# Optimization experiments

Hardware: AMD Instinct MI355X
Metric: run time of the kernel (lower is better)

The kernel has to match this reference:

```python
import jax, jax.numpy as jnp
import numpy as np
from jax import lax

N, M, T, V, C_IN, C_OUT, KT, PAD = 16, 2, 300, 25, 64, 64, 9, 4
BN_EPS = 1e-5

# NTU-RGB+D 25-joint skeleton edges (0-indexed), symmetric, plus self-loops
_NTU_EDGES = [(0,1),(1,20),(2,20),(3,2),(4,20),(5,4),(6,5),(7,6),(8,20),(9,8),
              (10,9),(11,10),(12,0),(13,12),(14,13),(15,14),(16,0),(17,16),
              (18,17),(19,18),(21,22),(22,7),(23,24),(24,11)]

def _build_adj():
    A = np.zeros((V, V), dtype=np.float32)
    for i, j in _NTU_EDGES:
        A[i, j] = 1.0
        A[j, i] = 1.0
    A += np.eye(V, dtype=np.float32)  # self-loops (DGL GCN preprocessing)
    return jnp.asarray(A)


def setup_inputs() -> dict:
    key = jax.random.key(0)
    ks = jax.random.split(key, 8)
    stdv = 1.0 / np.sqrt(C_OUT)
    # conv_init: normal(0, sqrt(2/(out_channels*prod(kernel))))
    conv_std = np.sqrt(2.0 / (C_OUT * KT * 1))
    return {
        "h": jax.random.normal(ks[0], (N * M * T * V, C_IN), dtype=jnp.float32),
        "adj": _build_adj(),
        "gcn_w": jax.random.uniform(ks[1], (C_IN, C_OUT), minval=-stdv, maxval=stdv, dtype=jnp.float32),
        "gcn_b": jax.random.uniform(ks[2], (C_OUT,), minval=-stdv, maxval=stdv, dtype=jnp.float32),
        "conv_w": conv_std * jax.random.normal(ks[3], (C_OUT, C_OUT, KT, 1), dtype=jnp.float32),
        "conv_b": jnp.zeros((C_OUT,), dtype=jnp.float32),
        "bn_gamma": jnp.ones((C_OUT,), dtype=jnp.float32),
        "bn_beta": jnp.zeros((C_OUT,), dtype=jnp.float32),
        "bn_mean": 0.1 * jax.random.normal(ks[4], (C_OUT,), dtype=jnp.float32),
        "bn_var": jax.random.uniform(ks[5], (C_OUT,), minval=0.5, maxval=1.5, dtype=jnp.float32),
    }


def reference(h, adj, gcn_w, gcn_b, conv_w, conv_b, bn_gamma, bn_beta, bn_mean, bn_var):
    # ---- GCNLayer (dropout is identity at eval) ----
    # symmetric norm = deg^{-1/2}, identical across the N*M*T copies of the skeleton
    norm = adj.sum(axis=1) ** -0.5                      # (V,)
    x = h @ gcn_w                                        # (N*M*T*V, C_OUT)
    x = x.reshape(-1, V, C_OUT) * norm[:, None]          # pre-norm scale
    x = jnp.einsum('vu,buc->bvc', adj, x)                # copy_src + sum aggregation
    x = x * norm[:, None] + gcn_b                        # post-norm scale + bias
    x = jax.nn.relu(x)

    # ---- TemporalConvNetwork ----
    v = x.reshape(N, M, T, V, C_OUT)
    v = v.transpose(0, 1, 4, 2, 3).reshape(N * M, C_OUT, T, V)   # (NM, C, T, V)
    v = lax.conv_general_dilated(v, conv_w, window_strides=(1, 1),
                                 padding=[(PAD, PAD), (0, 0)],
                                 dimension_numbers=('NCHW', 'OIHW', 'NCHW'))
    v = v + conv_b[None, :, None, None]
    inv_std = bn_gamma / jnp.sqrt(bn_var + BN_EPS)       # eval-mode BatchNorm2d
    v = (v - bn_mean[None, :, None, None]) * inv_std[None, :, None, None] + bn_beta[None, :, None, None]
    v = jax.nn.relu(v)
    v = v.reshape(N, M, C_OUT, T, V).transpose(0, 1, 3, 4, 2)    # (N, M, T, V, C)

    # ---- residual (downt is None since in_feats == out_feats and stride == 1) ----
    return v + h.reshape(N, M, T, V, C_IN)
```

## Files before the change

kernel.cpp:

```cpp
#include <hip/hip_runtime.h>
#include <hip/hip_bf16.h>


typedef __bf16 bf16x8 __attribute__((ext_vector_type(8)));
typedef __bf16 bf16x4 __attribute__((ext_vector_type(4)));
typedef float  f32x4  __attribute__((ext_vector_type(4)));

#define Y_OFF   0
#define WC2_OFF 30720000
#define WGT_OFF 30793728
#define A2P_OFF 30801920
#define SC_OFF  30803968
#define SH_OFF  30804224

__global__ __launch_bounds__(256) void prep_kernel(
    const float* __restrict__ adj, const float* __restrict__ gcn_w,
    const float* __restrict__ conv_w, const float* __restrict__ conv_b,
    const float* __restrict__ bn_g, const float* __restrict__ bn_b,
    const float* __restrict__ bn_m, const float* __restrict__ bn_v,
    __bf16* __restrict__ wc2, __bf16* __restrict__ wgt,
    __bf16* __restrict__ a2p, float* __restrict__ scale, float* __restrict__ shift) {
  int tid = threadIdx.x;
  for (int e = blockIdx.x * 256 + tid; e < 36864; e += gridDim.x * 256) {
    int j = e & 7, t1 = e >> 3, c = t1 & 63, g = t1 >> 6;
    int kap = g * 8 + j, kt = kap >> 6, ci = kap & 63;
    wc2[e] = (__bf16)conv_w[(c * 64 + ci) * 9 + kt];
  }
  if (blockIdx.x == 0) {
    for (int e = tid; e < 4096; e += 256) {
      int c = e >> 6, k = e & 63;
      wgt[e] = (__bf16)gcn_w[k * 64 + c];
    }
  } else if (blockIdx.x == 1) {
    for (int e = tid; e < 1024; e += 256) {
      int v = e >> 5, u = e & 31;
      float val = 0.f;
      if (v < 25 && u < 25) {
        float dv = 0.f, du = 0.f;
        for (int t = 0; t < 25; ++t) { dv += adj[v * 25 + t]; du += adj[u * 25 + t]; }
        val = rsqrtf(dv) * adj[v * 25 + u] * rsqrtf(du);
      }
      a2p[e] = (__bf16)val;
    }
  } else if (blockIdx.x == 2) {
    if (tid < 64) {
      float sc = bn_g[tid] * rsqrtf(bn_v[tid] + 1e-5f);
      scale[tid] = sc;
      shift[tid] = (conv_b[tid] - bn_m[tid]) * sc + bn_b[tid];
    }
  }
}

__global__ __launch_bounds__(64) void gcn_kernel(
    const float* __restrict__ h, const __bf16* __restrict__ wgt_g,
    const __bf16* __restrict__ a2p_g, const float* __restrict__ gcn_b,
    __bf16* __restrict__ y) {
  __shared__ __align__(16) __bf16 hb[2048];
  __shared__ __align__(16) __bf16 x1t[64 * 40];
  int lane = threadIdx.x;
  int l15 = lane & 15, quad = lane >> 4;
  int skel = blockIdx.x;
  int nm = skel / 300, tloc = skel - nm * 300;

  bf16x8 awg[4][2];
  for (int mt = 0; mt < 4; ++mt)
    for (int kk = 0; kk < 2; ++kk)
      awg[mt][kk] = *(const bf16x8*)&wgt_g[(mt * 16 + l15) * 64 + kk * 32 + quad * 8];
  bf16x8 ba[2];
  for (int nt = 0; nt < 2; ++nt)
    ba[nt] = *(const bf16x8*)&a2p_g[(nt * 16 + l15) * 32 + quad * 8];

  if (lane < 56) *(uint4*)&hb[1600 + lane * 8] = (uint4){0u, 0u, 0u, 0u};
  for (int it = 0; it < 7; ++it) {
    int u = it * 4 + quad;
    if (u < 25) {
      float4 hv = *(const float4*)&h[(skel * 25 + u) * 64 + l15 * 4];
      bf16x4 b4; b4[0] = (__bf16)hv.x; b4[1] = (__bf16)hv.y; b4[2] = (__bf16)hv.z; b4[3] = (__bf16)hv.w;
      int ch = l15 >> 1;
      *(bf16x4*)&hb[u * 64 + (((ch ^ (u & 7)) * 8) | ((l15 & 1) * 4))] = b4;
    }
  }
  for (int mt = 0; mt < 4; ++mt)
    for (int nt = 0; nt < 2; ++nt) {
      f32x4 acc = {0.f, 0.f, 0.f, 0.f};
      int u = nt * 16 + l15;
      for (int kk = 0; kk < 2; ++kk) {
        bf16x8 b = *(const bf16x8*)&hb[u * 64 + (((kk * 4 + quad) ^ (u & 7)) * 8)];
        acc = __builtin_amdgcn_mfma_f32_16x16x32_bf16(awg[mt][kk], b, acc, 0, 0, 0);
      }
      int c0 = mt * 16 + quad * 4;
      for (int r = 0; r < 4; ++r) x1t[(c0 + r) * 40 + u] = (__bf16)acc[r];
    }
  for (int mt = 0; mt < 4; ++mt)
    for (int nt = 0; nt < 2; ++nt) {
      f32x4 acc = {0.f, 0.f, 0.f, 0.f};
      bf16x8 a = *(const bf16x8*)&x1t[(mt * 16 + l15) * 40 + quad * 8];
      acc = __builtin_amdgcn_mfma_f32_16x16x32_bf16(a, ba[nt], acc, 0, 0, 0);
      int v = nt * 16 + l15, c0 = mt * 16 + quad * 4;
      if (v < 25) {
        float4 bias = *(const float4*)&gcn_b[c0];
        bf16x4 o;
        o[0] = (__bf16)fmaxf(acc[0] + bias.x, 0.f);
        o[1] = (__bf16)fmaxf(acc[1] + bias.y, 0.f);
        o[2] = (__bf16)fmaxf(acc[2] + bias.z, 0.f);
        o[3] = (__bf16)fmaxf(acc[3] + bias.w, 0.f);
        int ch = (c0 >> 3) ^ (v & 7);
        *(bf16x4*)&hb[v * 64 + ((ch * 8) | (c0 & 7))] = o;
      }
    }
  for (int e = lane; e < 200; e += 64) {
    int v = e >> 3, ch = e & 7;
    uint4 val = *(const uint4*)&hb[v * 64 + ((ch ^ (v & 7)) * 8)];
    *(uint4*)&y[((nm * 25 + v) * 300 + tloc) * 64 + ch * 8] = val;
  }
}

__global__ __launch_bounds__(256, 8) void conv_kernel(
    const __bf16* __restrict__ y, const __bf16* __restrict__ wc2,
    const float* __restrict__ scale, const float* __restrict__ shift,
    const float* __restrict__ h, float* __restrict__ out) {
  __shared__ __align__(16) __bf16 my[72 * 64];
  int tid = threadIdx.x, w = tid >> 6, lane = tid & 63;
  int l15 = lane & 15, quad = lane >> 4;
  int ti = blockIdx.x, vv = blockIdx.y, nm = blockIdx.z;
  int t0 = (ti < 4) ? ti * 64 : 236;

  {
    const __bf16* ybase = &y[((nm * 25 + vv) * 300) * 64];
    uint4 stg[3];
    for (int it = 0; it < 3; ++it) {
      int idx = it * 256 + tid;
      uint4 val = {0u, 0u, 0u, 0u};
      if (idx < 576) {
        int r = idx >> 3, ch = idx & 7, tg = t0 - 4 + r;
        if (tg >= 0 && tg < 300) val = *(const uint4*)&ybase[tg * 64 + ch * 8];
      }
      stg[it] = val;
    }
    for (int it = 0; it < 3; ++it) {
      int idx = it * 256 + tid;
      if (idx < 576) {
        int r = idx >> 3, ch = idx & 7;
        *(uint4*)&my[r * 64 + ((ch ^ (r & 7)) * 8)] = stg[it];
      }
    }
  }
  __syncthreads();

  f32x4 acc[4];
  for (int n = 0; n < 4; ++n) acc[n] = (f32x4){0.f, 0.f, 0.f, 0.f};

  bf16x8 a0, a1;
#define LOADA(dst, kk_) dst = *(const bf16x8*)&wc2[((((kk_) * 4 + quad) * 64) + w * 16 + l15) * 8];
#define COMPUTE(kk_, areg) { int kt = (kk_) >> 1, chb = ((kk_) & 1) * 4 + quad; \
    for (int n = 0; n < 4; ++n) { \
      int row = n * 16 + l15 + kt; \
      bf16x8 b = *(const bf16x8*)&my[row * 64 + ((chb ^ (row & 7)) * 8)]; \
      acc[n] = __builtin_amdgcn_mfma_f32_16x16x32_bf16(areg, b, acc[n], 0, 0, 0); \
    } }
  LOADA(a0, 0)
  for (int kk = 0; kk < 18; kk += 2) {
    LOADA(a1, kk + 1)
    COMPUTE(kk, a0)
    if (kk + 2 < 18) LOADA(a0, kk + 2)
    COMPUTE(kk + 1, a1)
  }
#undef LOADA
#undef COMPUTE

  int c0 = w * 16 + quad * 4;
  float4 sc = *(const float4*)&scale[c0];
  float4 sh = *(const float4*)&shift[c0];
  for (int n = 0; n < 4; ++n) {
    int tt = t0 + n * 16 + l15;
    int idx = ((nm * 300 + tt) * 25 + vv) * 64 + c0;
    float4 hr = *(const float4*)&h[idx];
    float4 o;
    o.x = fmaxf(acc[n][0] * sc.x + sh.x, 0.f) + hr.x;
    o.y = fmaxf(acc[n][1] * sc.y + sh.y, 0.f) + hr.y;
    o.z = fmaxf(acc[n][2] * sc.z + sh.z, 0.f) + hr.z;
    o.w = fmaxf(acc[n][3] * sc.w + sh.w, 0.f) + hr.w;
    *(float4*)&out[idx] = o;
  }
}

extern "C" void kernel_launch(void* const* d_in, const int* in_sizes, int n_in,
                              void* d_out, int out_size, void* d_ws, size_t ws_size,
                              hipStream_t stream) {
  const float* h      = (const float*)d_in[0];
  const float* adj    = (const float*)d_in[1];
  const float* gcn_w  = (const float*)d_in[2];
  const float* gcn_b  = (const float*)d_in[3];
  const float* conv_w = (const float*)d_in[4];
  const float* conv_b = (const float*)d_in[5];
  const float* bn_g   = (const float*)d_in[6];
  const float* bn_b   = (const float*)d_in[7];
  const float* bn_m   = (const float*)d_in[8];
  const float* bn_v   = (const float*)d_in[9];
  float* out = (float*)d_out;
  char* ws = (char*)d_ws;

  __bf16* y_ws   = (__bf16*)(ws + Y_OFF);
  __bf16* wc2    = (__bf16*)(ws + WC2_OFF);
  __bf16* wgt    = (__bf16*)(ws + WGT_OFF);
  __bf16* a2p    = (__bf16*)(ws + A2P_OFF);
  float*  scale  = (float*)(ws + SC_OFF);
  float*  shift  = (float*)(ws + SH_OFF);

  prep_kernel<<<64, 256, 0, stream>>>(adj, gcn_w, conv_w, conv_b, bn_g, bn_b, bn_m, bn_v,
                                      wc2, wgt, a2p, scale, shift);
  gcn_kernel<<<9600, 64, 0, stream>>>(h, wgt, a2p, gcn_b, y_ws);
  conv_kernel<<<dim3(5, 25, 32), 256, 0, stream>>>(y_ws, wc2, scale, shift, h, out);
}
```

Measured before the change: 173.8 us.

## Switch temporal conv to 32x32x16 MFMA tiles with two waves per block

Rewrites the temporal conv kernel to use 32x32x16 bf16 MFMA instead of 16x16x32. Each block now runs two waves instead of four, and each wave computes 32 channels by 64 timesteps. The packed conv weight layout in the prep kernel is reordered to match the new A-operand fragment. The aim is fewer MFMA issues and fewer LDS B-fragment reads per output, at the cost of more accumulator registers per thread and fewer threads per block for staging loads. The epilogue now writes strided float4 groups of channels, which changes how the global accesses coalesce.

```diff
diff --git a/kernel.cpp b/kernel.cpp
--- a/kernel.cpp
+++ b/kernel.cpp
@@ -5,6 +5,7 @@
 typedef __bf16 bf16x8 __attribute__((ext_vector_type(8)));
 typedef __bf16 bf16x4 __attribute__((ext_vector_type(4)));
 typedef float  f32x4  __attribute__((ext_vector_type(4)));
+typedef float  f32x16 __attribute__((ext_vector_type(16)));
 
 #define Y_OFF   0
 #define WC2_OFF 30720000
@@ -23,7 +24,8 @@
   int tid = threadIdx.x;
   for (int e = blockIdx.x * 256 + tid; e < 36864; e += gridDim.x * 256) {
     int j = e & 7, t1 = e >> 3, c = t1 & 63, g = t1 >> 6;
-    int kap = g * 8 + j, kt = kap >> 6, ci = kap & 63;
+    int kt = g >> 3, ks = (g >> 1) & 3, hi = g & 1;
+    int ci = ks * 16 + hi * 8 + j;
     wc2[e] = (__bf16)conv_w[(c * 64 + ci) * 9 + kt];
   }
   if (blockIdx.x == 0) {
@@ -115,21 +117,41 @@
   }
 }
 
-__global__ __launch_bounds__(256, 8) void conv_kernel(
+__device__ __forceinline__ void conv_epilogue(
+    const f32x16& a, int tt, int nm, int vv, int cbase,
+    const float* __restrict__ scale, const float* __restrict__ shift,
+    const float* __restrict__ h, float* __restrict__ out) {
+  int base = ((nm * 300 + tt) * 25 + vv) * 64 + cbase;
+#pragma unroll
+  for (int q = 0; q < 4; ++q) {
+    int idx = base + q * 8;
+    float4 hr = *(const float4*)&h[idx];
+    float4 s4 = *(const float4*)&scale[cbase + q * 8];
+    float4 h4 = *(const float4*)&shift[cbase + q * 8];
+    float4 o;
+    o.x = fmaxf(a[q * 4 + 0] * s4.x + h4.x, 0.f) + hr.x;
+    o.y = fmaxf(a[q * 4 + 1] * s4.y + h4.y, 0.f) + hr.y;
+    o.z = fmaxf(a[q * 4 + 2] * s4.z + h4.z, 0.f) + hr.z;
+    o.w = fmaxf(a[q * 4 + 3] * s4.w + h4.w, 0.f) + hr.w;
+    *(float4*)&out[idx] = o;
+  }
+}
+
+__global__ __launch_bounds__(128, 4) void conv_kernel(
     const __bf16* __restrict__ y, const __bf16* __restrict__ wc2,
     const float* __restrict__ scale, const float* __restrict__ shift,
     const float* __restrict__ h, float* __restrict__ out) {
   __shared__ __align__(16) __bf16 my[72 * 64];
-  int tid = threadIdx.x, w = tid >> 6, lane = tid & 63;
-  int l15 = lane & 15, quad = lane >> 4;
+  int tid = threadIdx.x, ct = tid >> 6, lane = tid & 63;
+  int l31 = lane & 31, hi = lane >> 5;
   int ti = blockIdx.x, vv = blockIdx.y, nm = blockIdx.z;
   int t0 = (ti < 4) ? ti * 64 : 236;
 
   {
     const __bf16* ybase = &y[((nm * 25 + vv) * 300) * 64];
-    uint4 stg[3];
-    for (int it = 0; it < 3; ++it) {
-      int idx = it * 256 + tid;
+    uint4 stg[5];
+    for (int it = 0; it < 5; ++it) {
+      int idx = it * 128 + tid;
       uint4 val = {0u, 0u, 0u, 0u};
       if (idx < 576) {
         int r = idx >> 3, ch = idx & 7, tg = t0 - 4 + r;
@@ -137,8 +159,8 @@
       }
       stg[it] = val;
     }
-    for (int it = 0; it < 3; ++it) {
-      int idx = it * 256 + tid;
+    for (int it = 0; it < 5; ++it) {
+      int idx = it * 128 + tid;
       if (idx < 576) {
         int r = idx >> 3, ch = idx & 7;
         *(uint4*)&my[r * 64 + ((ch ^ (r & 7)) * 8)] = stg[it];
@@ -147,41 +169,36 @@
   }
   __syncthreads();
 
-  f32x4 acc[4];
-  for (int n = 0; n < 4; ++n) acc[n] = (f32x4){0.f, 0.f, 0.f, 0.f};
-
-  bf16x8 a0, a1;
-#define LOADA(dst, kk_) dst = *(const bf16x8*)&wc2[((((kk_) * 4 + quad) * 64) + w * 16 + l15) * 8];
-#define COMPUTE(kk_, areg) { int kt = (kk_) >> 1, chb = ((kk_) & 1) * 4 + quad; \
-    for (int n = 0; n < 4; ++n) { \
-      int row = n * 16 + l15 + kt; \
-      bf16x8 b = *(const bf16x8*)&my[row * 64 + ((chb ^ (row & 7)) * 8)]; \
-      acc[n] = __builtin_amdgcn_mfma_f32_16x16x32_bf16(areg, b, acc[n], 0, 0, 0); \
-    } }
-  LOADA(a0, 0)
-  for (int kk = 0; kk < 18; kk += 2) {
-    LOADA(a1, kk + 1)
-    COMPUTE(kk, a0)
-    if (kk + 2 < 18) LOADA(a0, kk + 2)
-    COMPUTE(kk + 1, a1)
-  }
-#undef LOADA
-#undef COMPUTE
-
-  int c0 = w * 16 + quad * 4;
-  float4 sc = *(const float4*)&scale[c0];
-  float4 sh = *(const float4*)&shift[c0];
-  for (int n = 0; n < 4; ++n) {
-    int tt = t0 + n * 16 + l15;
-    int idx = ((nm * 300 + tt) * 25 + vv) * 64 + c0;
-    float4 hr = *(const float4*)&h[idx];
-    float4 o;
-    o.x = fmaxf(acc[n][0] * sc.x + sh.x, 0.f) + hr.x;
-    o.y = fmaxf(acc[n][1] * sc.y + sh.y, 0.f) + hr.y;
-    o.z = fmaxf(acc[n][2] * sc.z + sh.z, 0.f) + hr.z;
-    o.w = fmaxf(acc[n][3] * sc.w + sh.w, 0.f) + hr.w;
-    *(float4*)&out[idx] = o;
-  }
+  f32x16 acc0 = {0.f, 0.f, 0.f, 0.f, 0.f, 0.f, 0.f, 0.f,
+                 0.f, 0.f, 0.f, 0.f, 0.f, 0.f, 0.f, 0.f};
+  f32x16 acc1 = {0.f, 0.f, 0.f, 0.f, 0.f, 0.f, 0.f, 0.f,
+                 0.f, 0.f, 0.f, 0.f, 0.f, 0.f, 0.f, 0.f};
+
+  const __bf16* aptr = wc2 + (hi * 64 + ct * 32 + l31) * 8;
+#define BPTR(s_) (&my[(l31 + ((s_) >> 2)) * 64 + \
+                      (((((s_) & 3) * 2 + hi) ^ ((l31 + ((s_) >> 2)) & 7)) * 8)])
+
+  bf16x8 a0 = *(const bf16x8*)aptr, a1;
+#pragma unroll
+  for (int s = 0; s < 36; s += 2) {
+    a1 = *(const bf16x8*)(aptr + (s + 1) * 1024);
+    const __bf16* bp = BPTR(s);
+    bf16x8 b0 = *(const bf16x8*)bp;
+    bf16x8 b1 = *(const bf16x8*)(bp + 2048);
+    acc0 = __builtin_amdgcn_mfma_f32_32x32x16_bf16(a0, b0, acc0, 0, 0, 0);
+    acc1 = __builtin_amdgcn_mfma_f32_32x32x16_bf16(a0, b1, acc1, 0, 0, 0);
+    if (s + 2 < 36) a0 = *(const bf16x8*)(aptr + (s + 2) * 1024);
+    bp = BPTR(s + 1);
+    b0 = *(const bf16x8*)bp;
+    b1 = *(const bf16x8*)(bp + 2048);
+    acc0 = __builtin_amdgcn_mfma_f32_32x32x16_bf16(a1, b0, acc0, 0, 0, 0);
+    acc1 = __builtin_amdgcn_mfma_f32_32x32x16_bf16(a1, b1, acc1, 0, 0, 0);
+  }
+#undef BPTR
+
+  int cbase = ct * 32 + hi * 4;
+  conv_epilogue(acc0, t0 + l31,      nm, vv, cbase, scale, shift, h, out);
+  conv_epilogue(acc1, t0 + 32 + l31, nm, vv, cbase, scale, shift, h, out);
 }
 
 extern "C" void kernel_launch(void* const* d_in, const int* in_sizes, int n_in,
@@ -210,5 +227,5 @@
   prep_kernel<<<64, 256, 0, stream>>>(adj, gcn_w, conv_w, conv_b, bn_g, bn_b, bn_m, bn_v,
                                       wc2, wgt, a2p, scale, shift);
   gcn_kernel<<<9600, 64, 0, stream>>>(h, wgt, a2p, gcn_b, y_ws);
-  conv_kernel<<<dim3(5, 25, 32), 256, 0, stream>>>(y_ws, wc2, scale, shift, h, out);
-}
+  conv_kernel<<<dim3(5, 25, 32), 128, 0, stream>>>(y_ws, wc2, scale, shift, h, out);
+}
```

After: 177.2 us. Within noise of the previous version (+2.0%).

## Make conv kernel persistent with double-buffered async LDS staging and register-resident weights

Applied to the files above, without the earlier changes.

The conv kernel becomes a persistent grid of 1024 blocks, each looping over a contiguous range of (time-tile, joint, nm) work items. It double-buffers the LDS tile and prefetches the next item with global_load_lds while computing the current one. The swizzle moves from the LDS write to the global source address. All 18 weight fragments are loaded once into registers, which removes repeated weight loads but raises register pressure and halves the occupancy target in launch bounds.

```diff
diff --git a/kernel.cpp b/kernel.cpp
--- a/kernel.cpp
+++ b/kernel.cpp
@@ -115,72 +115,87 @@
   }
 }
 
-__global__ __launch_bounds__(256, 8) void conv_kernel(
+__device__ __forceinline__ void conv_decode(int item, int& t0, int& nm, int& vv) {
+  int ti = item % 5, rest = item / 5;
+  vv = rest % 25; nm = rest / 25;
+  t0 = (ti < 4) ? ti * 64 : 236;
+}
+
+__global__ __launch_bounds__(256, 4) void conv_kernel(
     const __bf16* __restrict__ y, const __bf16* __restrict__ wc2,
     const float* __restrict__ scale, const float* __restrict__ shift,
     const float* __restrict__ h, float* __restrict__ out) {
-  __shared__ __align__(16) __bf16 my[72 * 64];
+  __shared__ __align__(16) __bf16 my[2][72 * 64];
   int tid = threadIdx.x, w = tid >> 6, lane = tid & 63;
   int l15 = lane & 15, quad = lane >> 4;
-  int ti = blockIdx.x, vv = blockIdx.y, nm = blockIdx.z;
-  int t0 = (ti < 4) ? ti * 64 : 236;
-
-  {
+
+  bf16x8 awc[18];
+#pragma unroll
+  for (int kk = 0; kk < 18; ++kk)
+    awc[kk] = *(const bf16x8*)&wc2[(((kk * 4 + quad) * 64) + w * 16 + l15) * 8];
+
+  int start = (blockIdx.x * 125) >> 5;
+  int end   = ((blockIdx.x + 1) * 125) >> 5;
+
+  auto stage = [&](int item, int b) {
+    int t0, nm, vv; conv_decode(item, t0, nm, vv);
     const __bf16* ybase = &y[((nm * 25 + vv) * 300) * 64];
-    uint4 stg[3];
+#pragma unroll
     for (int it = 0; it < 3; ++it) {
-      int idx = it * 256 + tid;
-      uint4 val = {0u, 0u, 0u, 0u};
-      if (idx < 576) {
+      int wbase = it * 256 + (tid & 192);
+      if (wbase < 576) {
+        int idx = wbase + lane;
         int r = idx >> 3, ch = idx & 7, tg = t0 - 4 + r;
-        if (tg >= 0 && tg < 300) val = *(const uint4*)&ybase[tg * 64 + ch * 8];
-      }
-      stg[it] = val;
-    }
-    for (int it = 0; it < 3; ++it) {
-      int idx = it * 256 + tid;
-      if (idx < 576) {
-        int r = idx >> 3, ch = idx & 7;
-        *(uint4*)&my[r * 64 + ((ch ^ (r & 7)) * 8)] = stg[it];
-      }
-    }
-  }
-  __syncthreads();
-
-  f32x4 acc[4];
-  for (int n = 0; n < 4; ++n) acc[n] = (f32x4){0.f, 0.f, 0.f, 0.f};
-
-  bf16x8 a0, a1;
-#define LOADA(dst, kk_) dst = *(const bf16x8*)&wc2[((((kk_) * 4 + quad) * 64) + w * 16 + l15) * 8];
-#define COMPUTE(kk_, areg) { int kt = (kk_) >> 1, chb = ((kk_) & 1) * 4 + quad; \
-    for (int n = 0; n < 4; ++n) { \
-      int row = n * 16 + l15 + kt; \
-      bf16x8 b = *(const bf16x8*)&my[row * 64 + ((chb ^ (row & 7)) * 8)]; \
-      acc[n] = __builtin_amdgcn_mfma_f32_16x16x32_bf16(areg, b, acc[n], 0, 0, 0); \
-    } }
-  LOADA(a0, 0)
-  for (int kk = 0; kk < 18; kk += 2) {
-    LOADA(a1, kk + 1)
-    COMPUTE(kk, a0)
-    if (kk + 2 < 18) LOADA(a0, kk + 2)
-    COMPUTE(kk + 1, a1)
-  }
-#undef LOADA
-#undef COMPUTE
-
-  int c0 = w * 16 + quad * 4;
-  float4 sc = *(const float4*)&scale[c0];
-  float4 sh = *(const float4*)&shift[c0];
-  for (int n = 0; n < 4; ++n) {
-    int tt = t0 + n * 16 + l15;
-    int idx = ((nm * 300 + tt) * 25 + vv) * 64 + c0;
-    float4 hr = *(const float4*)&h[idx];
-    float4 o;
-    o.x = fmaxf(acc[n][0] * sc.x + sh.x, 0.f) + hr.x;
-    o.y = fmaxf(acc[n][1] * sc.y + sh.y, 0.f) + hr.y;
-    o.z = fmaxf(acc[n][2] * sc.z + sh.z, 0.f) + hr.z;
-    o.w = fmaxf(acc[n][3] * sc.w + sh.w, 0.f) + hr.w;
-    *(float4*)&out[idx] = o;
+        __bf16* ldsb = &my[b][wbase * 8];
+        if (tg >= 0 && tg < 300) {
+          const __bf16* src = &ybase[tg * 64 + ((ch ^ (r & 7)) * 8)];
+          __builtin_amdgcn_global_load_lds(
+              (const __attribute__((address_space(1))) void*)src,
+              (__attribute__((address_space(3))) void*)ldsb, 16, 0, 0);
+        } else {
+          *(uint4*)&my[b][idx * 8] = (uint4){0u, 0u, 0u, 0u};
+        }
+      }
+    }
+  };
+
+  int b = 0;
+  stage(start, 0);
+  for (int item = start; item < end; ++item) {
+    __syncthreads();
+    if (item + 1 < end) stage(item + 1, b ^ 1);
+    int t0, nm, vv; conv_decode(item, t0, nm, vv);
+
+    f32x4 acc[4];
+#pragma unroll
+    for (int n = 0; n < 4; ++n) acc[n] = (f32x4){0.f, 0.f, 0.f, 0.f};
+#pragma unroll
+    for (int kk = 0; kk < 18; ++kk) {
+      int kt = kk >> 1, chb = (kk & 1) * 4 + quad;
+#pragma unroll
+      for (int n = 0; n < 4; ++n) {
+        int row = n * 16 + l15 + kt;
+        bf16x8 bfr = *(const bf16x8*)&my[b][row * 64 + ((chb ^ (row & 7)) * 8)];
+        acc[n] = __builtin_amdgcn_mfma_f32_16x16x32_bf16(awc[kk], bfr, acc[n], 0, 0, 0);
+      }
+    }
+
+    int c0 = w * 16 + quad * 4;
+    float4 sc = *(const float4*)&scale[c0];
+    float4 sh = *(const float4*)&shift[c0];
+#pragma unroll
+    for (int n = 0; n < 4; ++n) {
+      int tt = t0 + n * 16 + l15;
+      int idx = ((nm * 300 + tt) * 25 + vv) * 64 + c0;
+      float4 hr = *(const float4*)&h[idx];
+      float4 o;
+      o.x = fmaxf(acc[n][0] * sc.x + sh.x, 0.f) + hr.x;
+      o.y = fmaxf(acc[n][1] * sc.y + sh.y, 0.f) + hr.y;
+      o.z = fmaxf(acc[n][2] * sc.z + sh.z, 0.f) + hr.z;
+      o.w = fmaxf(acc[n][3] * sc.w + sh.w, 0.f) + hr.w;
+      *(float4*)&out[idx] = o;
+    }
+    b ^= 1;
   }
 }
 
@@ -210,5 +225,5 @@
   prep_kernel<<<64, 256, 0, stream>>>(adj, gcn_w, conv_w, conv_b, bn_g, bn_b, bn_m, bn_v,
                                       wc2, wgt, a2p, scale, shift);
   gcn_kernel<<<9600, 64, 0, stream>>>(h, wgt, a2p, gcn_b, y_ws);
-  conv_kernel<<<dim3(5, 25, 32), 256, 0, stream>>>(y_ws, wc2, scale, shift, h, out);
-}
+  conv_kernel<<<1024, 256, 0, stream>>>(y_ws, wc2, scale, shift, h, out);
+}
```

Measured after the change: 181.3 us. 4.3% more time.

## Process two conv tiles per block with double-buffered LDS prefetch

Applied to the files above, without the earlier changes.

Each conv block now handles two (t-tile, joint, nm) work items, loading the second tile's input from global into registers while MFMAs run on the first tile, then staging it into a second LDS buffer. The grid shrinks from 4000 to 2000 blocks, and the loops are fully unrolled. The aim is to hide global load latency behind compute. In exchange, LDS per block doubles and occupancy is lowered to 6 blocks per CU, and fewer blocks may leave some CUs idle.

```diff
diff --git a/kernel.cpp b/kernel.cpp
--- a/kernel.cpp
+++ b/kernel.cpp
@@ -115,73 +115,123 @@
   }
 }
 
-__global__ __launch_bounds__(256, 8) void conv_kernel(
+#define CONV_KLOOP(b_, acc_)                                                          \
+  {                                                                                   \
+    _Pragma("unroll")                                                                 \
+    for (int n = 0; n < 4; ++n) acc_[n] = (f32x4){0.f, 0.f, 0.f, 0.f};                \
+    bf16x8 a0, a1;                                                                    \
+    a0 = *(const bf16x8*)&wc2[((0 * 4 + quad) * 64 + w * 16 + l15) * 8];              \
+    _Pragma("unroll")                                                                 \
+    for (int kk = 0; kk < 18; kk += 2) {                                              \
+      a1 = *(const bf16x8*)&wc2[(((kk + 1) * 4 + quad) * 64 + w * 16 + l15) * 8];     \
+      { int kt = kk >> 1, chb = quad;                                                 \
+        _Pragma("unroll")                                                             \
+        for (int n = 0; n < 4; ++n) {                                                 \
+          int row = n * 16 + l15 + kt;                                                \
+          bf16x8 bb = *(const bf16x8*)&my[b_][row * 64 + ((chb ^ (row & 7)) * 8)];    \
+          acc_[n] = __builtin_amdgcn_mfma_f32_16x16x32_bf16(a0, bb, acc_[n], 0, 0, 0);\
+        } }                                                                           \
+      if (kk + 2 < 18) a0 = *(const bf16x8*)&wc2[(((kk + 2) * 4 + quad) * 64 + w * 16 + l15) * 8]; \
+      { int kt = kk >> 1, chb = 4 + quad;                                             \
+        _Pragma("unroll")                                                             \
+        for (int n = 0; n < 4; ++n) {                                                 \
+          int row = n * 16 + l15 + kt;                                                \
+          bf16x8 bb = *(const bf16x8*)&my[b_][row * 64 + ((chb ^ (row & 7)) * 8)];    \
+          acc_[n] = __builtin_amdgcn_mfma_f32_16x16x32_bf16(a1, bb, acc_[n], 0, 0, 0);\
+        } }                                                                           \
+    }                                                                                 \
+  }
+
+#define CONV_EPILOGUE(acc_, t0_, vv_, nm_)                                            \
+  {                                                                                   \
+    int c0 = w * 16 + quad * 4;                                                       \
+    float4 sc = *(const float4*)&scale[c0];                                           \
+    float4 sh = *(const float4*)&shift[c0];                                           \
+    _Pragma("unroll")                                                                 \
+    for (int n = 0; n < 4; ++n) {                                                     \
+      int tt = (t0_) + n * 16 + l15;                                                  \
+      int idx = (((nm_) * 300 + tt) * 25 + (vv_)) * 64 + c0;                          \
+      float4 hr = *(const float4*)&h[idx];                                            \
+      float4 o;                                                                       \
+      o.x = fmaxf(acc_[n][0] * sc.x + sh.x, 0.f) + hr.x;                              \
+      o.y = fmaxf(acc_[n][1] * sc.y + sh.y, 0.f) + hr.y;                              \
+      o.z = fmaxf(acc_[n][2] * sc.z + sh.z, 0.f) + hr.z;                              \
+      o.w = fmaxf(acc_[n][3] * sc.w + sh.w, 0.f) + hr.w;                              \
+      *(float4*)&out[idx] = o;                                                        \
+    }                                                                                 \
+  }
+
+__global__ __launch_bounds__(256, 6) void conv_kernel(
     const __bf16* __restrict__ y, const __bf16* __restrict__ wc2,
     const float* __restrict__ scale, const float* __restrict__ shift,
     const float* __restrict__ h, float* __restrict__ out) {
-  __shared__ __align__(16) __bf16 my[72 * 64];
+  __shared__ __align__(16) __bf16 my[2][72 * 64];
   int tid = threadIdx.x, w = tid >> 6, lane = tid & 63;
   int l15 = lane & 15, quad = lane >> 4;
-  int ti = blockIdx.x, vv = blockIdx.y, nm = blockIdx.z;
-  int t0 = (ti < 4) ? ti * 64 : 236;
-
+
+  int e0 = blockIdx.x * 2, e1 = e0 + 1;
+  int t0a, vva, nma;
+  { int ti = e0 % 5, r = e0 / 5; vva = r % 25; nma = r / 25; t0a = (ti < 4) ? ti * 64 : 236; }
+  int t0b, vvb, nmb;
+  { int ti = e1 % 5, r = e1 / 5; vvb = r % 25; nmb = r / 25; t0b = (ti < 4) ? ti * 64 : 236; }
+
+  uint4 stg[3];
   {
-    const __bf16* ybase = &y[((nm * 25 + vv) * 300) * 64];
-    uint4 stg[3];
-    for (int it = 0; it < 3; ++it) {
-      int idx = it * 256 + tid;
-      uint4 val = {0u, 0u, 0u, 0u};
-      if (idx < 576) {
-        int r = idx >> 3, ch = idx & 7, tg = t0 - 4 + r;
-        if (tg >= 0 && tg < 300) val = *(const uint4*)&ybase[tg * 64 + ch * 8];
-      }
-      stg[it] = val;
-    }
+    const __bf16* yb = &y[((nma * 25 + vva) * 300) * 64];
+#pragma unroll
+    for (int it = 0; it < 3; ++it) {
+      int idx = it * 256 + tid;
+      uint4 v = {0u, 0u, 0u, 0u};
+      if (idx < 576) {
+        int r = idx >> 3, ch = idx & 7, tg = t0a - 4 + r;
+        if (tg >= 0 && tg < 300) v = *(const uint4*)&yb[tg * 64 + ch * 8];
+      }
+      stg[it] = v;
+    }
+#pragma unroll
     for (int it = 0; it < 3; ++it) {
       int idx = it * 256 + tid;
       if (idx < 576) {
         int r = idx >> 3, ch = idx & 7;
-        *(uint4*)&my[r * 64 + ((ch ^ (r & 7)) * 8)] = stg[it];
+        *(uint4*)&my[0][r * 64 + ((ch ^ (r & 7)) * 8)] = stg[it];
       }
     }
   }
   __syncthreads();
 
-  f32x4 acc[4];
-  for (int n = 0; n < 4; ++n) acc[n] = (f32x4){0.f, 0.f, 0.f, 0.f};
-
-  bf16x8 a0, a1;
-#define LOADA(dst, kk_) dst = *(const bf16x8*)&wc2[((((kk_) * 4 + quad) * 64) + w * 16 + l15) * 8];
-#define COMPUTE(kk_, areg) { int kt = (kk_) >> 1, chb = ((kk_) & 1) * 4 + quad; \
-    for (int n = 0; n < 4; ++n) { \
-      int row = n * 16 + l15 + kt; \
-      bf16x8 b = *(const bf16x8*)&my[row * 64 + ((chb ^ (row & 7)) * 8)]; \
-      acc[n] = __builtin_amdgcn_mfma_f32_16x16x32_bf16(areg, b, acc[n], 0, 0, 0); \
-    } }
-  LOADA(a0, 0)
-  for (int kk = 0; kk < 18; kk += 2) {
-    LOADA(a1, kk + 1)
-    COMPUTE(kk, a0)
-    if (kk + 2 < 18) LOADA(a0, kk + 2)
-    COMPUTE(kk + 1, a1)
-  }
-#undef LOADA
-#undef COMPUTE
-
-  int c0 = w * 16 + quad * 4;
-  float4 sc = *(const float4*)&scale[c0];
-  float4 sh = *(const float4*)&shift[c0];
-  for (int n = 0; n < 4; ++n) {
-    int tt = t0 + n * 16 + l15;
-    int idx = ((nm * 300 + tt) * 25 + vv) * 64 + c0;
-    float4 hr = *(const float4*)&h[idx];
-    float4 o;
-    o.x = fmaxf(acc[n][0] * sc.x + sh.x, 0.f) + hr.x;
-    o.y = fmaxf(acc[n][1] * sc.y + sh.y, 0.f) + hr.y;
-    o.z = fmaxf(acc[n][2] * sc.z + sh.z, 0.f) + hr.z;
-    o.w = fmaxf(acc[n][3] * sc.w + sh.w, 0.f) + hr.w;
-    *(float4*)&out[idx] = o;
-  }
+  {
+    const __bf16* yb = &y[((nmb * 25 + vvb) * 300) * 64];
+#pragma unroll
+    for (int it = 0; it < 3; ++it) {
+      int idx = it * 256 + tid;
+      uint4 v = {0u, 0u, 0u, 0u};
+      if (idx < 576) {
+        int r = idx >> 3, ch = idx & 7, tg = t0b - 4 + r;
+        if (tg >= 0 && tg < 300) v = *(const uint4*)&yb[tg * 64 + ch * 8];
+      }
+      stg[it] = v;
+    }
+  }
+
+  f32x4 accA[4];
+  CONV_KLOOP(0, accA)
+
+  {
+#pragma unroll
+    for (int it = 0; it < 3; ++it) {
+      int idx = it * 256 + tid;
+      if (idx < 576) {
+        int r = idx >> 3, ch = idx & 7;
+        *(uint4*)&my[1][r * 64 + ((ch ^ (r & 7)) * 8)] = stg[it];
+      }
+    }
+  }
+  __syncthreads();
+
+  CONV_EPILOGUE(accA, t0a, vva, nma)
+  f32x4 accB[4];
+  CONV_KLOOP(1, accB)
+  CONV_EPILOGUE(accB, t0b, vvb, nmb)
 }
 
 extern "C" void kernel_launch(void* const* d_in, const int* in_sizes, int n_in,
@@ -210,5 +260,5 @@
   prep_kernel<<<64, 256, 0, stream>>>(adj, gcn_w, conv_w, conv_b, bn_g, bn_b, bn_m, bn_v,
                                       wc2, wgt, a2p, scale, shift);
   gcn_kernel<<<9600, 64, 0, stream>>>(h, wgt, a2p, gcn_b, y_ws);
-  conv_kernel<<<dim3(5, 25, 32), 256, 0, stream>>>(y_ws, wc2, scale, shift, h, out);
-}
+  conv_kernel<<<2000, 256, 0, stream>>>(y_ws, wc2, scale, shift, h, out);
+}
```

Measured after the change: 185.2 us. 6.6% more time.
